# Kernel tuning notes

Measured on AMD Instinct MI355X. Metric: run time of the kernel, lower is better.

The kernel has to match this reference:

```python
import jax, jax.numpy as jnp
import numpy as np

B, S, D = 2, 2048, 2048
H = 16
HD = D // H  # 128
ROPE_BASE = 10000.0


def _rope_cos_sin(seq_len, head_dim):
    inv_freq = 1.0 / (ROPE_BASE ** (jnp.arange(0, head_dim, 2, dtype=jnp.float32) / head_dim))
    t = jnp.arange(seq_len, dtype=jnp.float32)
    freqs = jnp.einsum('i,j->ij', t, inv_freq)  # [S, HD/2]
    emb = jnp.concatenate([freqs, freqs], axis=-1)  # [S, HD]
    return jnp.cos(emb)[None, None], jnp.sin(emb)[None, None]  # [1,1,S,HD]


def _rotate_half(x):
    x1, x2 = jnp.split(x, 2, axis=-1)
    return jnp.concatenate([-x2, x1], axis=-1)


def setup_inputs() -> dict:
    key = jax.random.key(0)
    k1, k2, k3 = jax.random.split(key, 3)
    hidden_states = jax.random.normal(k1, (B, S, D), dtype=jnp.float32)
    w_qkv = jax.random.normal(k2, (D, 3 * D), dtype=jnp.float32) * (D ** -0.5)
    w_o = jax.random.normal(k3, (D, D), dtype=jnp.float32) * (D ** -0.5)
    return {"hidden_states": hidden_states, "w_qkv": w_qkv, "w_o": w_o}


def reference(hidden_states, w_qkv, w_o):
    b, s, _ = hidden_states.shape
    qkv = jnp.einsum('bsd,de->bse', hidden_states, w_qkv)  # [B,S,3D]
    q, k, v = jnp.split(qkv, 3, axis=-1)
    # [B,H,S,HD]
    q = q.reshape(b, s, H, HD).transpose(0, 2, 1, 3)
    k = k.reshape(b, s, H, HD).transpose(0, 2, 1, 3)
    v = v.reshape(b, s, H, HD).transpose(0, 2, 1, 3)
    cos, sin = _rope_cos_sin(s, HD)
    q = q * cos + _rotate_half(q) * sin
    k = k * cos + _rotate_half(k) * sin
    scale = 1.0 / np.sqrt(HD).astype(np.float32)
    scores = jnp.einsum('bhqd,bhkd->bhqk', q, k) * scale  # [B,H,S,S]
    causal = jnp.triu(jnp.ones((s, s), dtype=bool), k=1)
    scores = jnp.where(causal, -jnp.inf, scores)
    attn = jax.nn.softmax(scores, axis=-1)
    out = jnp.einsum('bhqk,bhkd->bhqd', attn, v)  # [B,H,S,HD]
    out = out.transpose(0, 2, 1, 3).reshape(b, s, H * HD)
    return jnp.einsum('bsd,de->bse', out, w_o)
```

## Files before the change

kernel.cpp:

```cpp
#include <hip/hip_runtime.h>
#include <math.h>

typedef unsigned short u16;
typedef short s16x8 __attribute__((ext_vector_type(8)));
typedef float f32x4 __attribute__((ext_vector_type(4)));

#define ATTN_SCALE 0.08838834764831845f
#define NEG_BIG -1.0e30f

__device__ __forceinline__ u16 f2bf(float f) {
  union { float f; unsigned u; } c; c.f = f;
  return (u16)((c.u + 0x7fffu + ((c.u >> 16) & 1u)) >> 16);
}
__device__ __forceinline__ float bf2f(u16 v) {
  union { unsigned u; float f; } c; c.u = ((unsigned)v) << 16;
  return c.f;
}
__device__ __forceinline__ f32x4 mfma16(s16x8 a, s16x8 b, f32x4 c) {
  return __builtin_amdgcn_mfma_f32_16x16x32_bf16(a, b, c, 0, 0, 0);
}
__device__ __forceinline__ void gl_lds16(const u16* g, u16* l) {
  __builtin_amdgcn_global_load_lds(
      (const __attribute__((address_space(1))) unsigned int*)g,
      (__attribute__((address_space(3))) unsigned int*)l, 16, 0, 0);
}

__global__ __launch_bounds__(256) void k_cast(const float* __restrict__ in,
                                              u16* __restrict__ out, int n4) {
  const int i = blockIdx.x * 256 + threadIdx.x;
  if (i >= n4) return;
  const float4 v = ((const float4*)in)[i];
  ushort4 o;
  o.x = f2bf(v.x); o.y = f2bf(v.y); o.z = f2bf(v.z); o.w = f2bf(v.w);
  ((ushort4*)out)[i] = o;
}

__global__ __launch_bounds__(256) void k_transpose_cast(const float* __restrict__ in,
                                                        u16* __restrict__ out,
                                                        int R, int C) {
  __shared__ __attribute__((aligned(16))) u16 tile[32][33];
  const int c0 = blockIdx.x * 32, r0 = blockIdx.y * 32;
  const int tx = threadIdx.x, ty = threadIdx.y;
#pragma unroll
  for (int i = 0; i < 4; ++i)
    tile[ty + 8 * i][tx] = f2bf(in[(r0 + ty + 8 * i) * C + c0 + tx]);
  __syncthreads();
#pragma unroll
  for (int i = 0; i < 4; ++i)
    out[(c0 + ty + 8 * i) * R + r0 + tx] = tile[tx][ty + 8 * i];
}

__global__ __launch_bounds__(256) void k_vtrans(const u16* __restrict__ qkv,
                                                u16* __restrict__ vt) {
  __shared__ __attribute__((aligned(16))) u16 tile[32][33];
  const int bh = blockIdx.z, b = bh >> 4, h = bh & 15;
  const int s0 = blockIdx.x * 32, d0 = blockIdx.y * 32;
  const int tx = threadIdx.x, ty = threadIdx.y;
#pragma unroll
  for (int i = 0; i < 4; ++i) {
    const int s = s0 + ty + 8 * i;
    tile[ty + 8 * i][tx] = qkv[(b * 2048 + s) * 6144 + 4096 + h * 128 + d0 + tx];
  }
  __syncthreads();
#pragma unroll
  for (int i = 0; i < 4; ++i) {
    const int d = d0 + ty + 8 * i;
    vt[bh * 262144 + d * 2048 + s0 + tx] = tile[tx][ty + 8 * i];
  }
}

__global__ __launch_bounds__(256) void k_rope(u16* __restrict__ qkv) {
  const int id = blockIdx.x * 256 + threadIdx.x;
  const int j = id & 63;
  const int h = (id >> 6) & 15;
  const int sec = (id >> 10) & 1;
  const int m = id >> 11;
  const int s = m & 2047;
  const int base = m * 6144 + sec * 2048 + h * 128 + j;
  const float q0 = bf2f(qkv[base]);
  const float q1 = bf2f(qkv[base + 64]);
  const float inv = exp2f((float)j * -0.20762050593046014f);
  const float ang = (float)s * inv;
  float c, sn;
  sincosf(ang, &sn, &c);
  qkv[base]      = f2bf(q0 * c - q1 * sn);
  qkv[base + 64] = f2bf(q1 * c + q0 * sn);
}

template <bool A_F32, typename OUT_T>
__global__ __launch_bounds__(256) void k_gemm_lds(const void* __restrict__ Ap, int lda,
                                                  const u16* __restrict__ BT,
                                                  OUT_T* __restrict__ C, int ldc,
                                                  int K) {
  __shared__ __attribute__((aligned(16))) u16 As[128 * 32];
  __shared__ __attribute__((aligned(16))) u16 Bs[128 * 32];
  const int tid = threadIdx.x;
  const int lane = tid & 63, wave = tid >> 6;
  const int lm = lane & 15, quad = lane >> 4;
  const int wm = wave >> 1, wn = wave & 1;
  const int m0 = blockIdx.y * 128, n0 = blockIdx.x * 128;
  const int srow = lane >> 2, scol = (lane & 3) * 8;

  const f32x4 fzero = {0.f, 0.f, 0.f, 0.f};
  f32x4 acc[4][4];
#pragma unroll
  for (int i = 0; i < 4; ++i)
#pragma unroll
    for (int j = 0; j < 4; ++j) acc[i][j] = fzero;

  for (int k0 = 0; k0 < K; k0 += 32) {
    __syncthreads();
    if constexpr (A_F32) {
      const float* Af = (const float*)Ap;
#pragma unroll
      for (int i = 0; i < 2; ++i) {
        const int seg = tid + 256 * i;
        const int row = seg >> 2, c8 = (seg & 3) * 8;
        const float4 u = *(const float4*)&Af[(m0 + row) * lda + k0 + c8];
        const float4 w = *(const float4*)&Af[(m0 + row) * lda + k0 + c8 + 4];
        uint4 pk;
        pk.x = (unsigned)f2bf(u.x) | ((unsigned)f2bf(u.y) << 16);
        pk.y = (unsigned)f2bf(u.z) | ((unsigned)f2bf(u.w) << 16);
        pk.z = (unsigned)f2bf(w.x) | ((unsigned)f2bf(w.y) << 16);
        pk.w = (unsigned)f2bf(w.z) | ((unsigned)f2bf(w.w) << 16);
        *(uint4*)&As[row * 32 + c8] = pk;
      }
#pragma unroll
      for (int j = 0; j < 2; ++j) {
        const int rb = wave * 32 + j * 16;
        gl_lds16(&BT[(n0 + rb + srow) * K + k0 + scol], &Bs[rb * 32]);
      }
    } else {
      const u16* Ab = (const u16*)Ap;
#pragma unroll
      for (int j = 0; j < 2; ++j) {
        const int rb = wave * 32 + j * 16;
        gl_lds16(&Ab[(m0 + rb + srow) * lda + k0 + scol], &As[rb * 32]);
        gl_lds16(&BT[(n0 + rb + srow) * K + k0 + scol], &Bs[rb * 32]);
      }
    }
    __syncthreads();

    s16x8 af[4], bfr[4];
#pragma unroll
    for (int t = 0; t < 4; ++t) {
      af[t]  = *(const s16x8*)&As[(wm * 64 + t * 16 + lm) * 32 + quad * 8];
      bfr[t] = *(const s16x8*)&Bs[(wn * 64 + t * 16 + lm) * 32 + quad * 8];
    }
#pragma unroll
    for (int mt = 0; mt < 4; ++mt)
#pragma unroll
      for (int nt = 0; nt < 4; ++nt)
        acc[mt][nt] = mfma16(af[mt], bfr[nt], acc[mt][nt]);
  }
#pragma unroll
  for (int mt = 0; mt < 4; ++mt)
#pragma unroll
    for (int nt = 0; nt < 4; ++nt)
#pragma unroll
      for (int r = 0; r < 4; ++r) {
        const float v = acc[mt][nt][r];
        const int idx = (m0 + wm * 64 + mt * 16 + quad * 4 + r) * ldc +
                        n0 + wn * 64 + nt * 16 + lm;
        if constexpr (sizeof(OUT_T) == 2) C[idx] = f2bf(v);
        else                              C[idx] = v;
      }
}

__global__ __launch_bounds__(256) void k_attn(u16* __restrict__ qkv,
                                              const u16* __restrict__ vt) {
  __shared__ __attribute__((aligned(16))) u16 Ks[2][64 * 128];
  __shared__ __attribute__((aligned(16))) u16 Vs[2][128 * 64];
  __shared__ __attribute__((aligned(16))) u16 Ps[4 * 16 * 72];
  const int bh = blockIdx.x, pair = blockIdx.y;
  const int b = bh >> 4, h = bh & 15;
  const int tid = threadIdx.x;
  const int lane = tid & 63, wave = tid >> 6;
  const int lm = lane & 15, quad = lane >> 4;
  const int pbase = wave * 1152;
  const int sw = lm & 7;
  const f32x4 fzero = {0.f, 0.f, 0.f, 0.f};

  const int phase_end = pair;

  auto dma_tile = [&](int kt0, int buf) {
#pragma unroll
    for (int i = 0; i < 4; ++i) {
      const int row = i * 16 + wave * 4 + (lane >> 4);
      const int cc = (lane & 15) ^ (row & 7);
      gl_lds16(&qkv[(b * 2048 + kt0 + row) * 6144 + 2048 + h * 128 + cc * 8],
               &Ks[buf][(i * 16 + wave * 4) * 128]);
    }
#pragma unroll
    for (int i = 0; i < 4; ++i) {
      const int row = i * 32 + wave * 8 + (lane >> 3);
      const int cc = (lane & 7) ^ (row & 7);
      gl_lds16(&vt[bh * 262144 + row * 2048 + kt0 + cc * 8],
               &Vs[buf][(i * 32 + wave * 8) * 64]);
    }
  };

  dma_tile(0, 0);

  int qtile = pair;
  int qb = qtile * 64;
  int qrow = qb + wave * 16 + lm;
  int qoff = (b * 2048 + qrow) * 6144 + h * 128;
  s16x8 qfrag[4];
#pragma unroll
  for (int c = 0; c < 4; ++c)
    qfrag[c] = *(const s16x8*)&qkv[qoff + c * 32 + quad * 8];
  f32x4 o[8];
#pragma unroll
  for (int dt = 0; dt < 8; ++dt) o[dt] = fzero;
  float m_run = NEG_BIG, l_run = 0.f;

  __syncthreads();

  for (int it = 0; it < 33; ++it) {
    const int kt0 = (it <= phase_end ? it : it - phase_end - 1) * 64;
    const int buf = it & 1;

    if (it < 32) {
      const int nkt = (it + 1 <= phase_end ? it + 1 : it - phase_end) * 64;
      dma_tile(nkt, buf ^ 1);
    }

    f32x4 sa[4];
#pragma unroll
    for (int ss = 0; ss < 4; ++ss) sa[ss] = fzero;
#pragma unroll
    for (int ss = 0; ss < 4; ++ss)
#pragma unroll
      for (int c = 0; c < 4; ++c) {
        const int ccs = (c * 4 + quad) ^ sw;
        s16x8 a = *(const s16x8*)&Ks[buf][(ss * 16 + lm) * 128 + ccs * 8];
        sa[ss] = mfma16(a, qfrag[c], sa[ss]);
      }

    float p[4][4];
    float vmax = NEG_BIG;
#pragma unroll
    for (int ss = 0; ss < 4; ++ss)
#pragma unroll
      for (int r = 0; r < 4; ++r) {
        const int kg = kt0 + ss * 16 + quad * 4 + r;
        float v = sa[ss][r] * ATTN_SCALE;
        if (kg > qrow) v = NEG_BIG;
        p[ss][r] = v;
        vmax = fmaxf(vmax, v);
      }
    vmax = fmaxf(vmax, __shfl_xor(vmax, 16, 64));
    vmax = fmaxf(vmax, __shfl_xor(vmax, 32, 64));
    const float m_new = fmaxf(m_run, vmax);
    const float alpha = __expf(m_run - m_new);
    float rsum = 0.f;
#pragma unroll
    for (int ss = 0; ss < 4; ++ss)
#pragma unroll
      for (int r = 0; r < 4; ++r) {
        p[ss][r] = __expf(p[ss][r] - m_new);
        rsum += p[ss][r];
      }
    rsum += __shfl_xor(rsum, 16, 64);
    rsum += __shfl_xor(rsum, 32, 64);
    l_run = l_run * alpha + rsum;
    m_run = m_new;
#pragma unroll
    for (int dt = 0; dt < 8; ++dt) o[dt] *= alpha;

#pragma unroll
    for (int ss = 0; ss < 4; ++ss)
#pragma unroll
      for (int r = 0; r < 4; ++r)
        Ps[pbase + lm * 72 + ss * 16 + quad * 4 + r] = f2bf(p[ss][r]);
    const s16x8 pv0 = *(const s16x8*)&Ps[pbase + lm * 72 + quad * 8];
    const s16x8 pv1 = *(const s16x8*)&Ps[pbase + lm * 72 + 32 + quad * 8];

#pragma unroll
    for (int dt = 0; dt < 8; ++dt) {
      const int c0 = (quad ^ sw) * 8, c1 = ((4 + quad) ^ sw) * 8;
      s16x8 a0 = *(const s16x8*)&Vs[buf][(dt * 16 + lm) * 64 + c0];
      s16x8 a1 = *(const s16x8*)&Vs[buf][(dt * 16 + lm) * 64 + c1];
      o[dt] = mfma16(a1, pv1, mfma16(a0, pv0, o[dt]));
    }

    if (it == phase_end) {
      const float inv_l = 1.0f / l_run;
#pragma unroll
      for (int dt = 0; dt < 8; ++dt)
#pragma unroll
        for (int r = 0; r < 4; ++r)
          qkv[qoff + dt * 16 + quad * 4 + r] = f2bf(o[dt][r] * inv_l);
      qtile = 31 - pair;
      qb = qtile * 64;
      qrow = qb + wave * 16 + lm;
      qoff = (b * 2048 + qrow) * 6144 + h * 128;
#pragma unroll
      for (int c = 0; c < 4; ++c)
        qfrag[c] = *(const s16x8*)&qkv[qoff + c * 32 + quad * 8];
#pragma unroll
      for (int dt = 0; dt < 8; ++dt) o[dt] = fzero;
      m_run = NEG_BIG; l_run = 0.f;
    }

    if (it < 32) __syncthreads();
  }

  const float inv_l = 1.0f / l_run;
#pragma unroll
  for (int dt = 0; dt < 8; ++dt)
#pragma unroll
    for (int r = 0; r < 4; ++r)
      qkv[qoff + dt * 16 + quad * 4 + r] = f2bf(o[dt][r] * inv_l);
}

extern "C" void kernel_launch(void* const* d_in, const int* in_sizes, int n_in,
                              void* d_out, int out_size, void* d_ws, size_t ws_size,
                              hipStream_t stream) {
  const float* hidden = (const float*)d_in[0];
  const float* w_qkv  = (const float*)d_in[1];
  const float* w_o    = (const float*)d_in[2];
  float* out = (float*)d_out;
  u16* ws = (u16*)d_ws;

  u16* qkv   = ws;
  u16* wqkvT = ws + 25165824;
  u16* vt    = ws + 25165824;
  u16* woT   = ws + 33554432;
  u16* hb    = ws + 37748736;
  const bool fast = ws_size >= (size_t)46137344 * 2;

  dim3 tb(32, 8);
  k_transpose_cast<<<dim3(192, 64), tb, 0, stream>>>(w_qkv, wqkvT, 2048, 6144);
  if (fast) {
    k_cast<<<8192, 256, 0, stream>>>(hidden, hb, 2097152);
    k_gemm_lds<false, u16><<<dim3(48, 32), 256, 0, stream>>>(hb, 2048, wqkvT,
                                                             qkv, 6144, 2048);
  } else {
    k_gemm_lds<true, u16><<<dim3(48, 32), 256, 0, stream>>>(hidden, 2048, wqkvT,
                                                            qkv, 6144, 2048);
  }
  k_rope<<<32768, 256, 0, stream>>>(qkv);
  k_vtrans<<<dim3(64, 4, 32), tb, 0, stream>>>(qkv, vt);
  k_transpose_cast<<<dim3(64, 64), tb, 0, stream>>>(w_o, woT, 2048, 2048);
  k_attn<<<dim3(32, 16), 256, 0, stream>>>(qkv, vt);
  k_gemm_lds<false, float><<<dim3(16, 32), 256, 0, stream>>>(qkv, 6144, woT,
                                                             out, 2048, 2048);
}
```

Baseline: 439.4 us.

## Add 256x256-tile double-buffered GEMM for QKV projection

Adds a dedicated QKV-projection GEMM that uses 256x256 output tiles with 512 threads. It double-buffers K-chunks in LDS through direct global-to-LDS loads, XOR-swizzles the LDS layout, remaps block IDs across XCDs, and raises wave priority around the MFMA bursts. The larger tiles give more operand reuse per LDS load and fewer global loads than the previous 128x128 kernel. The cost is much higher register pressure from 32 accumulator fragments per wave, and only 384 blocks, which may leave parts of the GPU underfilled.

```diff
diff --git a/kernel.cpp b/kernel.cpp
--- a/kernel.cpp
+++ b/kernel.cpp
@@ -167,6 +167,91 @@
       }
 }
 
+__global__ __launch_bounds__(512, 2) void k_gemm256(const u16* __restrict__ A,
+                                                    const u16* __restrict__ BT,
+                                                    u16* __restrict__ C, int ldc) {
+  __shared__ __attribute__((aligned(16))) u16 As[2][2][256 * 32];
+  __shared__ __attribute__((aligned(16))) u16 Bs[2][2][256 * 32];
+  const int K = 2048;
+  const int tid = threadIdx.x;
+  const int lane = tid & 63, wave = tid >> 6;
+  const int lm = lane & 15, quad = lane >> 4;
+  const int wm = wave >> 2, wn = wave & 3;
+
+  int bid = (blockIdx.x & 7) * (gridDim.x >> 3) + (blockIdx.x >> 3);
+  const int m0 = (bid & 15) * 256;
+  const int n0 = (bid >> 4) * 256;
+
+  auto stage_half = [&](int kt, int kc, int bi) {
+    const int k0 = kt * 64 + kc * 32;
+#pragma unroll
+    for (int i = 0; i < 2; ++i) {
+      const int r = i * 128 + 16 * wave + (lane >> 2);
+      const int gc = (lane & 3) ^ (r & 3);
+      gl_lds16(&A[(m0 + r) * K + k0 + gc * 8],
+               &As[bi][kc][(i * 128 + 16 * wave) * 32]);
+      gl_lds16(&BT[(n0 + r) * K + k0 + gc * 8],
+               &Bs[bi][kc][(i * 128 + 16 * wave) * 32]);
+    }
+  };
+
+  const f32x4 fzero = {0.f, 0.f, 0.f, 0.f};
+  f32x4 acc[8][4];
+#pragma unroll
+  for (int i = 0; i < 8; ++i)
+#pragma unroll
+    for (int j = 0; j < 4; ++j) acc[i][j] = fzero;
+
+  stage_half(0, 0, 0);
+  stage_half(0, 1, 0);
+
+  for (int t = 0; t < 32; ++t) {
+    const int b = t & 1;
+#pragma unroll
+    for (int kc = 0; kc < 2; ++kc) {
+      if (t == 31 && kc == 1) {
+        asm volatile("s_waitcnt vmcnt(0)" ::: "memory");
+      } else {
+        asm volatile("s_waitcnt vmcnt(4)" ::: "memory");
+      }
+      asm volatile("s_barrier" ::: "memory");
+
+      if (t < 31) stage_half(t + 1, kc, b ^ 1);
+
+      s16x8 bfrag[4], afrag[8];
+#pragma unroll
+      for (int nt = 0; nt < 4; ++nt) {
+        const int r = wn * 64 + nt * 16 + lm;
+        const int cc = quad ^ (r & 3);
+        bfrag[nt] = *(const s16x8*)&Bs[b][kc][r * 32 + cc * 8];
+      }
+#pragma unroll
+      for (int mt = 0; mt < 8; ++mt) {
+        const int r = wm * 128 + mt * 16 + lm;
+        const int cc = quad ^ (r & 3);
+        afrag[mt] = *(const s16x8*)&As[b][kc][r * 32 + cc * 8];
+      }
+
+      __builtin_amdgcn_s_setprio(1);
+#pragma unroll
+      for (int mt = 0; mt < 8; ++mt)
+#pragma unroll
+        for (int nt = 0; nt < 4; ++nt)
+          acc[mt][nt] = mfma16(afrag[mt], bfrag[nt], acc[mt][nt]);
+      __builtin_amdgcn_s_setprio(0);
+    }
+  }
+
+#pragma unroll
+  for (int mt = 0; mt < 8; ++mt)
+#pragma unroll
+    for (int nt = 0; nt < 4; ++nt)
+#pragma unroll
+      for (int r = 0; r < 4; ++r)
+        C[(m0 + wm * 128 + mt * 16 + quad * 4 + r) * ldc +
+          n0 + wn * 64 + nt * 16 + lm] = f2bf(acc[mt][nt][r]);
+}
+
 __global__ __launch_bounds__(256) void k_attn(u16* __restrict__ qkv,
                                               const u16* __restrict__ vt) {
   __shared__ __attribute__((aligned(16))) u16 Ks[2][64 * 128];
@@ -335,8 +420,7 @@
   k_transpose_cast<<<dim3(192, 64), tb, 0, stream>>>(w_qkv, wqkvT, 2048, 6144);
   if (fast) {
     k_cast<<<8192, 256, 0, stream>>>(hidden, hb, 2097152);
-    k_gemm_lds<false, u16><<<dim3(48, 32), 256, 0, stream>>>(hb, 2048, wqkvT,
-                                                             qkv, 6144, 2048);
+    k_gemm256<<<384, 512, 0, stream>>>(hb, wqkvT, qkv, 6144);
   } else {
     k_gemm_lds<true, u16><<<dim3(48, 32), 256, 0, stream>>>(hidden, 2048, wqkvT,
                                                             qkv, 6144, 2048);
```

Result: slower. 454.6 us (+3.5%).
